# Kernel optimization log

Measured on AMD Instinct MI355X. Metric: run time of the kernel, lower is better.

Reference implementation:

```python
import jax, jax.numpy as jnp
import numpy as np

B, C_IN, T, H, W = 32, 1024, 7, 14, 14
C_INTER = 512


def setup_inputs() -> dict:
    key = jax.random.key(0)
    ks = jax.random.split(key, 8)
    s = lambda fan_in: 1.0 / np.sqrt(fan_in)
    return {
        "x_window": jax.random.normal(ks[0], (B, C_IN, T, H, W), jnp.float32),
        "nodes": jax.random.normal(ks[1], (T, C_INTER), jnp.float32),
        "Wq": jax.random.normal(ks[2], (C_IN, C_INTER), jnp.float32) * s(C_IN),
        "bq": jnp.zeros((C_INTER,), jnp.float32),
        "Wk": jax.random.normal(ks[3], (C_INTER, C_INTER), jnp.float32) * s(C_INTER),
        "bk": jnp.zeros((C_INTER,), jnp.float32),
        "Wv": jax.random.normal(ks[4], (C_IN, C_INTER), jnp.float32) * s(C_IN),
        "bv": jnp.zeros((C_INTER,), jnp.float32),
        "Wo": jax.random.normal(ks[5], (C_INTER, C_IN), jnp.float32) * s(C_INTER),
        "bo": jnp.zeros((C_IN,), jnp.float32),
    }


def reference(x_window, nodes, Wq, bq, Wk, bk, Wv, bv, Wo, bo):
    # x_window: (B, C_in, T, H, W); dropout is identity at eval time.
    t_mid = x_window.shape[2] // 2
    x_item = x_window[:, :, t_mid]                                   # (B, C_in, H, W)
    # pointwise (Linear3d) projections over channel dim
    query = jnp.einsum("bchw,cd->bdhw", x_item, Wq) + bq[None, :, None, None]
    key = nodes @ Wk + bk                                            # (T, C_inter)
    value = jnp.einsum("bcthw,cd->bdthw", x_window, Wv) + bv[None, :, None, None, None]
    # per-pixel attention scores over the T node keys
    alpha = jnp.einsum("bdhw,td->bthw", query, key)                  # (B, T, H, W)
    alpha = jax.nn.softmax(alpha, axis=1)
    # per-pixel weighted temporal sum
    y = jnp.einsum("bthw,bdthw->bdhw", alpha, value)                 # (B, C_inter, H, W)
    out = jnp.einsum("bdhw,dc->bchw", y, Wo) + bo[None, :, None, None]
    return out[:, :, None]                                           # (B, C_in, 1, H, W)
```

## Files before the change

kernel.cpp:

```cpp
#include <hip/hip_runtime.h>
#include <hip/hip_bf16.h>
#include <stdint.h>

#define BB    32
#define CIN   1024
#define TT    7
#define HHWW  196
#define HW4   49
#define CI    512
#define TMID  3
#define MM    (BB*HHWW)
#define NCH   16
#define CSZ   64

using bf16 = __hip_bfloat16;
typedef __attribute__((ext_vector_type(8))) short short8;
typedef __attribute__((ext_vector_type(4))) short s16x4;
typedef __attribute__((ext_vector_type(4))) float f32x4;

__device__ __forceinline__ void gload_lds16(const void* g, void* l) {
    __builtin_amdgcn_global_load_lds((const __attribute__((address_space(1))) void*)g,
                                     (__attribute__((address_space(3))) void*)l, 16, 0, 0);
}

template <int EPI>
__device__ __forceinline__ void gemm_body(const bf16* __restrict__ A, const bf16* __restrict__ Bt,
                                          void* __restrict__ Cout, const float* __restrict__ bias,
                                          int M, int N, int K, int bm, int bn,
                                          bf16* As, bf16* Bs) {
    int tid = threadIdx.x;
    int wid = tid >> 6, lane = tid & 63;
    int wr = wid >> 1, wc = wid & 1;
    f32x4 acc[4][4] = {};
    const bf16* Ab = A + (size_t)bm * 128 * K;
    const bf16* Bb = Bt + (size_t)bn * 128 * K;
    int row = lane & 15;
    int sw = row & 7;

    auto stage = [&](int buf, int k0) {
        #pragma unroll
        for (int it = 0; it < 4; ++it) {
            int g = it * 256 + tid;
            int r = g >> 3;
            int src8 = (g & 7) ^ (r & 7);
            gload_lds16(Ab + (size_t)r * K + k0 + src8 * 8, &As[buf * 8192 + g * 8]);
            gload_lds16(Bb + (size_t)r * K + k0 + src8 * 8, &Bs[buf * 8192 + g * 8]);
        }
    };

    stage(0, 0);
    int cur = 0;
    for (int k0 = 0; k0 < K; k0 += 64) {
        if (k0 + 64 < K) {
            stage(cur ^ 1, k0 + 64);
            asm volatile("s_waitcnt vmcnt(8)" ::: "memory");
        } else {
            asm volatile("s_waitcnt vmcnt(0)" ::: "memory");
        }
        __builtin_amdgcn_s_barrier();
        bf16* Ac = &As[cur * 8192];
        bf16* Bc = &Bs[cur * 8192];
        #pragma unroll
        for (int kk = 0; kk < 2; ++kk) {
            int kb8 = kk * 4 + (lane >> 4);
            int rd8 = kb8 ^ sw;
            short8 a[4], b[4];
            #pragma unroll
            for (int mi = 0; mi < 4; ++mi) {
                int arow = wr * 64 + mi * 16 + row;
                a[mi] = *(const short8*)&Ac[(arow * 8 + rd8) * 8];
            }
            #pragma unroll
            for (int ni = 0; ni < 4; ++ni) {
                int brow = wc * 64 + ni * 16 + row;
                b[ni] = *(const short8*)&Bc[(brow * 8 + rd8) * 8];
            }
            #pragma unroll
            for (int mi = 0; mi < 4; ++mi)
                #pragma unroll
                for (int ni = 0; ni < 4; ++ni)
                    acc[mi][ni] = __builtin_amdgcn_mfma_f32_16x16x32_bf16(a[mi], b[ni], acc[mi][ni], 0, 0, 0);
        }
        __builtin_amdgcn_s_barrier();
        cur ^= 1;
    }

    int col_l = lane & 15, row_l = (lane >> 4) * 4;
    if constexpr (EPI == 0) {
        bf16* C = (bf16*)Cout;
        #pragma unroll
        for (int mi = 0; mi < 4; ++mi) {
            int row0 = bm * 128 + wr * 64 + mi * 16 + row_l;
            #pragma unroll
            for (int ni = 0; ni < 4; ++ni) {
                int col = bn * 128 + wc * 64 + ni * 16 + col_l;
                #pragma unroll
                for (int r = 0; r < 4; ++r)
                    C[(size_t)(row0 + r) * N + col] = __float2bfloat16(acc[mi][ni][r]);
            }
        }
    } else {
        float* Cf = (float*)Cout;
        #pragma unroll
        for (int ni = 0; ni < 4; ++ni) {
            int n = bn * 128 + wc * 64 + ni * 16 + col_l;
            float bz = bias[n];
            #pragma unroll
            for (int mi = 0; mi < 4; ++mi) {
                int m0 = bm * 128 + wr * 64 + mi * 16 + row_l;
                int b = m0 / HHWW;
                int hw0 = m0 - b * HHWW;
                f32x4 v = acc[mi][ni];
                v[0] += bz; v[1] += bz; v[2] += bz; v[3] += bz;
                *(f32x4*)&Cf[((size_t)b * CIN + n) * HHWW + hw0] = v;
            }
        }
    }
}

__device__ __forceinline__ void gemm0_small(const bf16* __restrict__ A, const bf16* __restrict__ Bt,
                                            bf16* __restrict__ C, int bm, int bn, char* smem) {
    bf16* As = (bf16*)smem;
    bf16* Bs = (bf16*)(smem + 8192);
    const int K = 512, N = 1024;
    int tid = threadIdx.x;
    int wid = tid >> 6, lane = tid & 63;
    int wr = wid >> 1, wc = wid & 1;
    f32x4 acc[2][2] = {};
    const bf16* Ab = A + (size_t)bm * 64 * K;
    const bf16* Bb = Bt + (size_t)bn * 64 * K;
    int row = lane & 15;
    int sw = row & 7;

    for (int k0 = 0; k0 < K; k0 += 64) {
        #pragma unroll
        for (int it = 0; it < 2; ++it) {
            int g = it * 256 + tid;
            int r = g >> 3;
            int src8 = (g & 7) ^ (r & 7);
            gload_lds16(Ab + (size_t)r * K + k0 + src8 * 8, &As[g * 8]);
            gload_lds16(Bb + (size_t)r * K + k0 + src8 * 8, &Bs[g * 8]);
        }
        __syncthreads();
        #pragma unroll
        for (int kk = 0; kk < 2; ++kk) {
            int kb8 = kk * 4 + (lane >> 4);
            int rd8 = kb8 ^ sw;
            short8 a[2], b[2];
            #pragma unroll
            for (int mi = 0; mi < 2; ++mi)
                a[mi] = *(const short8*)&As[((wr * 32 + mi * 16 + row) * 8 + rd8) * 8];
            #pragma unroll
            for (int ni = 0; ni < 2; ++ni)
                b[ni] = *(const short8*)&Bs[((wc * 32 + ni * 16 + row) * 8 + rd8) * 8];
            #pragma unroll
            for (int mi = 0; mi < 2; ++mi)
                #pragma unroll
                for (int ni = 0; ni < 2; ++ni)
                    acc[mi][ni] = __builtin_amdgcn_mfma_f32_16x16x32_bf16(a[mi], b[ni], acc[mi][ni], 0, 0, 0);
        }
        __syncthreads();
    }

    int col_l = lane & 15, row_l = (lane >> 4) * 4;
    #pragma unroll
    for (int mi = 0; mi < 2; ++mi) {
        int row0 = bm * 64 + wr * 32 + mi * 16 + row_l;
        #pragma unroll
        for (int ni = 0; ni < 2; ++ni) {
            int col = bn * 64 + wc * 32 + ni * 16 + col_l;
            #pragma unroll
            for (int r = 0; r < 4; ++r)
                C[(size_t)(row0 + r) * N + col] = __float2bfloat16(acc[mi][ni][r]);
        }
    }
}

__global__ __launch_bounds__(256) void k_prep1(
    const float* __restrict__ nodes, const float* __restrict__ Wk, const float* __restrict__ bk,
    float* __restrict__ key,
    const float* __restrict__ Wv, const float* __restrict__ Wo,
    bf16* __restrict__ Wv_bf, bf16* __restrict__ WoT_bf,
    const float* __restrict__ bv, const float* __restrict__ bo, float* __restrict__ bvo) {
    __shared__ __align__(16) float lds[64 * 65];
    int u = blockIdx.x, tid = threadIdx.x;
    if (u < 56) {
        int t = u >> 3, dc = u & 7;
        int d_l = tid & 63, q = tid >> 6;
        int d = dc * 64 + d_l;
        float acc = 0.f;
        const float* nr = nodes + t * CI;
        #pragma unroll 4
        for (int c = q * 128; c < q * 128 + 128; ++c)
            acc = fmaf(nr[c], Wk[(size_t)c * CI + d], acc);
        lds[q * 64 + d_l] = acc;
        __syncthreads();
        if (q == 0)
            key[t * CI + d] = lds[d_l] + lds[64 + d_l] + lds[128 + d_l] + lds[192 + d_l] + bk[d];
    } else if (u < 568) {
        int i4 = ((u - 56) * 256 + tid) * 4;
        f32x4 v = *(const f32x4*)&Wv[i4];
        s16x4 o;
        #pragma unroll
        for (int j = 0; j < 4; ++j) { bf16 h = __float2bfloat16(v[j]); o[j] = *(short*)&h; }
        *(s16x4*)&Wv_bf[i4] = o;
    } else if (u < 696) {
        int u3 = u - 568;
        int dt = u3 >> 4, ct = u3 & 15;
        int r0 = tid >> 6, c = tid & 63;
        #pragma unroll
        for (int k = 0; k < 16; ++k) {
            int r = k * 4 + r0;
            lds[r * 65 + c] = Wo[(size_t)(dt * 64 + r) * CIN + ct * 64 + c];
        }
        __syncthreads();
        #pragma unroll
        for (int k = 0; k < 16; ++k) {
            int r = k * 4 + r0;
            WoT_bf[(size_t)(ct * 64 + r) * CI + dt * 64 + c] = __float2bfloat16(lds[c * 65 + r]);
        }
    } else {
        int cp0 = (u - 696) * 32;
        int cp_l = tid & 31, dq = tid >> 5;
        float acc = 0.f;
        #pragma unroll 4
        for (int d = dq * 64; d < dq * 64 + 64; ++d)
            acc = fmaf(bv[d], Wo[(size_t)d * CIN + cp0 + cp_l], acc);
        lds[dq * 32 + cp_l] = acc;
        __syncthreads();
        if (dq == 0) {
            float v = bo[cp0 + cp_l];
            #pragma unroll
            for (int g = 0; g < 8; ++g) v += lds[g * 32 + cp_l];
            bvo[cp0 + cp_l] = v;
        }
    }
}

__global__ __launch_bounds__(256) void k_wqk(
    const float* __restrict__ Wq, const float* __restrict__ bq,
    const float* __restrict__ key, float* __restrict__ Wqk, float* __restrict__ bqk) {
    int c = blockIdx.x * 4 + (threadIdx.x >> 6);
    int lane = threadIdx.x & 63;
    if (c > CIN) return;
    const float* src = (c < CIN) ? (Wq + (size_t)c * CI) : bq;
    float acc[TT] = {};
    #pragma unroll 2
    for (int it = 0; it < CI / 64; ++it) {
        float w = src[it * 64 + lane];
        #pragma unroll
        for (int t = 0; t < TT; ++t) acc[t] = fmaf(w, key[t * CI + it * 64 + lane], acc[t]);
    }
    #pragma unroll
    for (int t = 0; t < TT; ++t) {
        float v = acc[t];
        for (int off = 32; off; off >>= 1) v += __shfl_down(v, off);
        if (lane == 0) { if (c < CIN) Wqk[c * 8 + t] = v; else bqk[t] = v; }
    }
}

__global__ __launch_bounds__(256) void k_alpha(const float* __restrict__ x,
                                               const float* __restrict__ Wqk,
                                               float* __restrict__ part) {
    __shared__ float wq_s[CSZ * 8];
    int ch = blockIdx.x, b = blockIdx.y;
    int tid = threadIdx.x;
    for (int i = tid; i < CSZ * 8; i += 256) wq_s[i] = Wqk[ch * CSZ * 8 + i];
    __syncthreads();
    if (tid < HHWW) {
        float acc[TT] = {};
        const float* xb = x + (size_t)(b * CIN + ch * CSZ) * TT * HHWW + TMID * HHWW + tid;
        #pragma unroll 8
        for (int c = 0; c < CSZ; ++c) {
            float v = xb[(size_t)c * TT * HHWW];
            #pragma unroll
            for (int t = 0; t < TT; ++t) acc[t] = fmaf(v, wq_s[c * 8 + t], acc[t]);
        }
        #pragma unroll
        for (int t = 0; t < TT; ++t)
            part[((size_t)(b * NCH + ch) * TT + t) * HHWW + tid] = acc[t];
    }
}

__global__ __launch_bounds__(256) void k_softmaxF(const float* __restrict__ part,
                                                  const float* __restrict__ bqk,
                                                  float* __restrict__ alphaF) {
    int b = blockIdx.x;
    int tid = threadIdx.x;
    if (tid >= HHWW) return;
    float s[TT];
    #pragma unroll
    for (int t = 0; t < TT; ++t) s[t] = bqk[t];
    #pragma unroll
    for (int ch = 0; ch < NCH; ++ch)
        #pragma unroll
        for (int t = 0; t < TT; ++t)
            s[t] += part[((size_t)(b * NCH + ch) * TT + t) * HHWW + tid];
    float mx = s[0];
    #pragma unroll
    for (int t = 1; t < TT; ++t) mx = fmaxf(mx, s[t]);
    float e[TT], sum = 0.f;
    #pragma unroll
    for (int t = 0; t < TT; ++t) { e[t] = __expf(s[t] - mx); sum += e[t]; }
    float inv = 1.f / sum;
    #pragma unroll
    for (int t = 0; t < TT; ++t) alphaF[(size_t)b * TT * HHWW + t * HHWW + tid] = e[t] * inv;
}

__global__ __launch_bounds__(256) void k_smxwg0(
    const float* __restrict__ x, const float* __restrict__ alphaF, bf16* __restrict__ xw,
    const bf16* __restrict__ WoT_bf, const bf16* __restrict__ Wv_bf, bf16* __restrict__ WvoT) {
    __shared__ __align__(16) char smem[18048];
    int bid = blockIdx.x, tid = threadIdx.x;
    if (bid < 256) {
        gemm0_small(WoT_bf, Wv_bf, WvoT, bid >> 4, bid & 15, smem);
        return;
    }
    float* al = (float*)smem;
    bf16* txp = (bf16*)(smem + 5504);
    int u = bid - 256;
    int c0 = (u & 31) * 32;
    int b = u >> 5;
    for (int i = tid; i < TT * HHWW; i += 256) al[i] = alphaF[(size_t)b * TT * HHWW + i];
    __syncthreads();
    const f32x4* xp = (const f32x4*)x;
    f32x4 acc[7] = {};
    #pragma unroll
    for (int t = 0; t < TT; ++t) {
        #pragma unroll
        for (int k = 0; k < 7; ++k) {
            int w = k * 256 + tid;
            if (k == 6 && w >= 1568) continue;
            int c_l = w / 49;
            int hw4 = w - c_l * 49;
            f32x4 a4 = *(const f32x4*)&al[t * HHWW + hw4 * 4];
            f32x4 xv = xp[((size_t)(b * CIN + c0 + c_l) * TT + t) * HW4 + hw4];
            acc[k] += a4 * xv;
        }
    }
    #pragma unroll
    for (int k = 0; k < 7; ++k) {
        int w = k * 256 + tid;
        if (k == 6 && w >= 1568) continue;
        int c_l = w / 49;
        int hw4 = w - c_l * 49;
        int v = (hw4 & 7) << 2;
        #pragma unroll
        for (int r = 0; r < 4; ++r)
            txp[(hw4 * 4 + r) * 32 + (c_l ^ v)] = __float2bfloat16(acc[k][r]);
    }
    __syncthreads();
    #pragma unroll
    for (int k = 0; k < 7; ++k) {
        int w = k * 256 + tid;
        if (k == 6 && w >= 1568) continue;
        int m = w >> 3, seg = w & 7;
        int v = ((m >> 2) & 7) << 2;
        s16x4 val = *(const s16x4*)&txp[m * 32 + ((seg * 4) ^ v)];
        *(s16x4*)&xw[(size_t)(b * HHWW + m) * CIN + c0 + seg * 4] = val;
    }
}

__global__ __launch_bounds__(256) void k_gemm1(const bf16* __restrict__ A, const bf16* __restrict__ Bt,
                                               float* __restrict__ C, const float* __restrict__ bias) {
    __shared__ __align__(16) bf16 As[2 * 128 * 64];
    __shared__ __align__(16) bf16 Bs[2 * 128 * 64];
    gemm_body<1>(A, Bt, (void*)C, bias, MM, CIN, CIN, blockIdx.x, blockIdx.y, As, Bs);
}

extern "C" void kernel_launch(void* const* d_in, const int* in_sizes, int n_in,
                              void* d_out, int out_size, void* d_ws, size_t ws_size,
                              hipStream_t stream) {
    const float* x     = (const float*)d_in[0];
    const float* nodes = (const float*)d_in[1];
    const float* Wq    = (const float*)d_in[2];
    const float* bq    = (const float*)d_in[3];
    const float* Wk    = (const float*)d_in[4];
    const float* bk    = (const float*)d_in[5];
    const float* Wv    = (const float*)d_in[6];
    const float* bv    = (const float*)d_in[7];
    const float* Wo    = (const float*)d_in[8];
    const float* bo    = (const float*)d_in[9];

    uint8_t* w = (uint8_t*)d_ws;
    size_t off = 0;
    auto alloc = [&](size_t bytes) -> void* {
        void* p = w + off;
        off = (off + bytes + 255) & ~(size_t)255;
        return p;
    };
    float* key    = (float*)alloc((size_t)TT * CI * 4);
    float* Wqk    = (float*)alloc((size_t)CIN * 8 * 4);
    float* bqk    = (float*)alloc(8 * 4);
    float* bvo    = (float*)alloc((size_t)CIN * 4);
    bf16*  Wv_bf  = (bf16*)alloc((size_t)CIN * CI * 2);
    bf16*  WoT_bf = (bf16*)alloc((size_t)CIN * CI * 2);
    bf16*  WvoT   = (bf16*)alloc((size_t)CIN * CIN * 2);
    float* part   = (float*)alloc((size_t)BB * NCH * TT * HHWW * 4);
    float* alphaF = (float*)alloc((size_t)BB * TT * HHWW * 4);
    bf16*  xw     = (bf16*)alloc((size_t)MM * CIN * 2);
    (void)ws_size;

    k_prep1<<<728, 256, 0, stream>>>(nodes, Wk, bk, key, Wv, Wo, Wv_bf, WoT_bf, bv, bo, bvo);
    k_wqk<<<257, 256, 0, stream>>>(Wq, bq, key, Wqk, bqk);
    k_alpha<<<dim3(NCH, BB), 256, 0, stream>>>(x, Wqk, part);
    k_softmaxF<<<BB, 256, 0, stream>>>(part, bqk, alphaF);
    k_smxwg0<<<1280, 256, 0, stream>>>(x, alphaF, xw, WoT_bf, Wv_bf, WvoT);
    k_gemm1<<<dim3(49, 8), 256, 0, stream>>>(xw, WvoT, (float*)d_out, bvo);
}
```

Measured before the change: 88.10 us.

## Fold softmax kernel into weighted-sum kernel with per-batch flag handoff

Removes the separate softmax launch by giving its work to 32 extra blocks inside the weighted-sum/Wvo GEMM kernel. Consumer blocks spin on a per-batch atomic flag until the matching softmax block has written alpha, and the flags are reset inside the preceding alpha kernel. This saves one launch and its tail bubble. In exchange it relies on the producer blocks (lower block ids) being scheduled before consumers to avoid deadlock, and spinning blocks hold CU slots while they wait.

```diff
diff --git a/kernel.cpp b/kernel.cpp
--- a/kernel.cpp
+++ b/kernel.cpp
@@ -21,6 +21,14 @@
 __device__ __forceinline__ void gload_lds16(const void* g, void* l) {
     __builtin_amdgcn_global_load_lds((const __attribute__((address_space(1))) void*)g,
                                      (__attribute__((address_space(3))) void*)l, 16, 0, 0);
+}
+
+__device__ __forceinline__ void ctr_set(int* p) {
+    __hip_atomic_store(p, 1, __ATOMIC_RELEASE, __HIP_MEMORY_SCOPE_AGENT);
+}
+__device__ __forceinline__ void ctr_wait1(int* p) {
+    while (__hip_atomic_load(p, __ATOMIC_ACQUIRE, __HIP_MEMORY_SCOPE_AGENT) < 1)
+        __builtin_amdgcn_s_sleep(2);
 }
 
 template <int EPI>
@@ -261,10 +269,12 @@
 
 __global__ __launch_bounds__(256) void k_alpha(const float* __restrict__ x,
                                                const float* __restrict__ Wqk,
-                                               float* __restrict__ part) {
+                                               float* __restrict__ part,
+                                               int* __restrict__ ctr) {
     __shared__ float wq_s[CSZ * 8];
     int ch = blockIdx.x, b = blockIdx.y;
     int tid = threadIdx.x;
+    if (ch == 0 && b == 0 && tid < 32) ctr[tid] = 0;
     for (int i = tid; i < CSZ * 8; i += 256) wq_s[i] = Wqk[ch * CSZ * 8 + i];
     __syncthreads();
     if (tid < HHWW) {
@@ -282,46 +292,50 @@
     }
 }
 
-__global__ __launch_bounds__(256) void k_softmaxF(const float* __restrict__ part,
-                                                  const float* __restrict__ bqk,
-                                                  float* __restrict__ alphaF) {
-    int b = blockIdx.x;
-    int tid = threadIdx.x;
-    if (tid >= HHWW) return;
-    float s[TT];
-    #pragma unroll
-    for (int t = 0; t < TT; ++t) s[t] = bqk[t];
-    #pragma unroll
-    for (int ch = 0; ch < NCH; ++ch)
-        #pragma unroll
-        for (int t = 0; t < TT; ++t)
-            s[t] += part[((size_t)(b * NCH + ch) * TT + t) * HHWW + tid];
-    float mx = s[0];
-    #pragma unroll
-    for (int t = 1; t < TT; ++t) mx = fmaxf(mx, s[t]);
-    float e[TT], sum = 0.f;
-    #pragma unroll
-    for (int t = 0; t < TT; ++t) { e[t] = __expf(s[t] - mx); sum += e[t]; }
-    float inv = 1.f / sum;
-    #pragma unroll
-    for (int t = 0; t < TT; ++t) alphaF[(size_t)b * TT * HHWW + t * HHWW + tid] = e[t] * inv;
-}
-
 __global__ __launch_bounds__(256) void k_smxwg0(
-    const float* __restrict__ x, const float* __restrict__ alphaF, bf16* __restrict__ xw,
-    const bf16* __restrict__ WoT_bf, const bf16* __restrict__ Wv_bf, bf16* __restrict__ WvoT) {
+    const float* __restrict__ x, const float* __restrict__ alphaF_ro, bf16* __restrict__ xw,
+    const bf16* __restrict__ WoT_bf, const bf16* __restrict__ Wv_bf, bf16* __restrict__ WvoT,
+    const float* __restrict__ part, const float* __restrict__ bqk, float* __restrict__ alphaF,
+    int* __restrict__ ctr) {
     __shared__ __align__(16) char smem[18048];
     int bid = blockIdx.x, tid = threadIdx.x;
     if (bid < 256) {
         gemm0_small(WoT_bf, Wv_bf, WvoT, bid >> 4, bid & 15, smem);
         return;
     }
+    if (bid < 288) {
+        int b = bid - 256;
+        if (tid < HHWW) {
+            float s[TT];
+            #pragma unroll
+            for (int t = 0; t < TT; ++t) s[t] = bqk[t];
+            #pragma unroll
+            for (int ch = 0; ch < NCH; ++ch)
+                #pragma unroll
+                for (int t = 0; t < TT; ++t)
+                    s[t] += part[((size_t)(b * NCH + ch) * TT + t) * HHWW + tid];
+            float mx = s[0];
+            #pragma unroll
+            for (int t = 1; t < TT; ++t) mx = fmaxf(mx, s[t]);
+            float e[TT], sum = 0.f;
+            #pragma unroll
+            for (int t = 0; t < TT; ++t) { e[t] = __expf(s[t] - mx); sum += e[t]; }
+            float inv = 1.f / sum;
+            #pragma unroll
+            for (int t = 0; t < TT; ++t) alphaF[(size_t)b * TT * HHWW + t * HHWW + tid] = e[t] * inv;
+        }
+        __syncthreads();
+        if (tid == 0) { __threadfence(); ctr_set(&ctr[b]); }
+        return;
+    }
     float* al = (float*)smem;
     bf16* txp = (bf16*)(smem + 5504);
-    int u = bid - 256;
+    int u = bid - 288;
     int c0 = (u & 31) * 32;
     int b = u >> 5;
-    for (int i = tid; i < TT * HHWW; i += 256) al[i] = alphaF[(size_t)b * TT * HHWW + i];
+    if (tid == 0) ctr_wait1(&ctr[b]);
+    __syncthreads();
+    for (int i = tid; i < TT * HHWW; i += 256) al[i] = alphaF_ro[(size_t)b * TT * HHWW + i];
     __syncthreads();
     const f32x4* xp = (const f32x4*)x;
     f32x4 acc[7] = {};
@@ -399,12 +413,12 @@
     float* part   = (float*)alloc((size_t)BB * NCH * TT * HHWW * 4);
     float* alphaF = (float*)alloc((size_t)BB * TT * HHWW * 4);
     bf16*  xw     = (bf16*)alloc((size_t)MM * CIN * 2);
+    int*   ctr    = (int*)alloc(64 * 4);
     (void)ws_size;
 
     k_prep1<<<728, 256, 0, stream>>>(nodes, Wk, bk, key, Wv, Wo, Wv_bf, WoT_bf, bv, bo, bvo);
     k_wqk<<<257, 256, 0, stream>>>(Wq, bq, key, Wqk, bqk);
-    k_alpha<<<dim3(NCH, BB), 256, 0, stream>>>(x, Wqk, part);
-    k_softmaxF<<<BB, 256, 0, stream>>>(part, bqk, alphaF);
-    k_smxwg0<<<1280, 256, 0, stream>>>(x, alphaF, xw, WoT_bf, Wv_bf, WvoT);
+    k_alpha<<<dim3(NCH, BB), 256, 0, stream>>>(x, Wqk, part, ctr);
+    k_smxwg0<<<1312, 256, 0, stream>>>(x, alphaF, xw, WoT_bf, Wv_bf, WvoT, part, bqk, alphaF, ctr);
     k_gemm1<<<dim3(49, 8), 256, 0, stream>>>(xw, WvoT, (float*)d_out, bvo);
 }
```

Result: slower. 118.5 us (+34.5%).
